# Performance work log

Measured on AMD Instinct MI355X. Metric: run time of the kernel, lower is better.

The kernel has to match this reference:

```python
import jax, jax.numpy as jnp
import numpy as np
import math

HIDDEN = 1024
HEADS = 16
HEAD_DIM = HIDDEN // HEADS
B, S = 4, 2048


def setup_inputs() -> dict:
    key = jax.random.key(0)
    ks = jax.random.split(key, 10)
    x = jax.random.normal(ks[0], (B, S, HIDDEN), dtype=jnp.float32)
    time_intervals = jax.random.uniform(ks[1], (B, S, S), dtype=jnp.float32)
    mask = jax.random.randint(ks[2], (B, 1, S, S), 0, 2, dtype=jnp.int32)
    scale = 1.0 / math.sqrt(HIDDEN)
    Wq = jax.random.normal(ks[3], (HIDDEN, HIDDEN), dtype=jnp.float32) * scale
    bq = jnp.zeros((HIDDEN,), dtype=jnp.float32)
    Wk = jax.random.normal(ks[4], (HIDDEN, HIDDEN), dtype=jnp.float32) * scale
    bk = jnp.zeros((HIDDEN,), dtype=jnp.float32)
    Wv = jax.random.normal(ks[5], (HIDDEN, HIDDEN), dtype=jnp.float32) * scale
    bv = jnp.zeros((HIDDEN,), dtype=jnp.float32)
    alpha = jnp.asarray(0.1, dtype=jnp.float32)
    return {"x": x, "time_intervals": time_intervals, "mask": mask,
            "Wq": Wq, "bq": bq, "Wk": Wk, "bk": bk, "Wv": Wv, "bv": bv,
            "alpha": alpha}


def reference(x, time_intervals, mask, Wq, bq, Wk, bk, Wv, bv, alpha):
    b, s, _ = x.shape
    # projections -> [b, heads, s, head_dim]
    def proj(W, bias):
        y = x @ W + bias
        return y.reshape(b, s, HEADS, HEAD_DIM).transpose(0, 2, 1, 3)
    Q = proj(Wq, bq)
    K = proj(Wk, bk)
    V = proj(Wv, bv)
    scores = jnp.einsum('bhqd,bhkd->bhqk', Q, K) / math.sqrt(HEAD_DIM)
    # additive time-decay bias, broadcast over heads
    scores = scores + (-jnp.abs(alpha)) * time_intervals[:, None, :, :]
    scores = jnp.where(mask == 0, jnp.float32(-1e9), scores)
    attn = jax.nn.softmax(scores, axis=-1)
    out = jnp.einsum('bhqk,bhkd->bhqd', attn, V)
    return out.transpose(0, 2, 1, 3).reshape(b, s, HIDDEN)
```

## Files before the change

kernel.cpp:

```cpp
#include <hip/hip_runtime.h>
#include <hip/hip_bf16.h>
#include <hip/hip_fp16.h>

#define BATCH 4
#define SEQ   2048
#define HID   1024
#define HEADS 16
#define HDIM  64
#define MROWS (BATCH * SEQ)
#define LOG2E 1.4426950408889634f
#define SCL   (LOG2E / 8.0f)

typedef _Float16 v8h __attribute__((ext_vector_type(8)));
typedef _Float16 v4h __attribute__((ext_vector_type(4)));
typedef _Float16 v2h __attribute__((ext_vector_type(2)));
typedef float    v4f __attribute__((ext_vector_type(4)));
typedef int      v4i __attribute__((ext_vector_type(4)));

#define MFMA16(a, b, c) __builtin_amdgcn_mfma_f32_16x16x32_f16((a), (b), (c), 0, 0, 0)
#define MFMA16K16(a, b, c) __builtin_amdgcn_mfma_f32_16x16x16f16((a), (b), (c), 0, 0, 0)

__device__ inline int pk2(float a, float b) {
    return __builtin_bit_cast(int, __builtin_amdgcn_cvt_pkrtz(a, b));
}

__device__ __forceinline__ void async16(const void* g, void* l) {
    __builtin_amdgcn_global_load_lds(
        (const __attribute__((address_space(1))) unsigned int*)g,
        (__attribute__((address_space(3))) unsigned int*)l, 16, 0, 0);
}

#define SWZ(row, chunk) (((row) * 64) + ((((chunk) ^ ((row) & 7))) * 8))

__global__ __launch_bounds__(256) void cvt_x(const float* __restrict__ x,
                                             _Float16* __restrict__ xb) {
    int i = blockIdx.x * 256 + threadIdx.x;
    const float4* xp = (const float4*)x;
    float4 a = xp[2 * i];
    float4 b = xp[2 * i + 1];
    v4i o;
    o[0] = pk2(a.x, a.y); o[1] = pk2(a.z, a.w);
    o[2] = pk2(b.x, b.y); o[3] = pk2(b.z, b.w);
    ((v4i*)xb)[i] = o;
}

__global__ __launch_bounds__(256) void transw(const float* __restrict__ W0,
                                              const float* __restrict__ W1,
                                              const float* __restrict__ W2,
                                              _Float16* __restrict__ Wt) {
    const float* W = (blockIdx.z == 0) ? W0 : (blockIdx.z == 1 ? W1 : W2);
    _Float16* dst = Wt + (size_t)blockIdx.z * HID * HID;
    __shared__ float t[32][33];
    int bx = blockIdx.x * 32, by = blockIdx.y * 32;
    int tx = threadIdx.x, ty = threadIdx.y;
#pragma unroll
    for (int i = 0; i < 4; i++)
        t[ty + i * 8][tx] = W[(size_t)(by + ty + i * 8) * HID + bx + tx];
    __syncthreads();
#pragma unroll
    for (int i = 0; i < 4; i++)
        dst[(size_t)(bx + ty + i * 8) * HID + by + tx] = (_Float16)t[tx][ty + i * 8];
}

__global__ __launch_bounds__(256) void mkbias(const float* __restrict__ tiv,
                                              const int* __restrict__ msk,
                                              const float* __restrict__ alphap,
                                              _Float16* __restrict__ biasT) {
    __shared__ _Float16 L[16 * 264];
    const int b = blockIdx.z, Q16 = blockIdx.y, kc0 = blockIdx.x * 256;
    const int tid = threadIdx.x;
    const float ca = -fabsf(alphap[0]) * LOG2E;
    const int prow = tid >> 6;
    const int pcol = (tid & 63) * 4;
#pragma unroll
    for (int pi = 0; pi < 4; pi++) {
        int r = pi * 4 + prow;
        size_t g = ((size_t)b * SEQ + Q16 * 16 + r) * SEQ + kc0 + pcol;
        float4 tv = *(const float4*)(tiv + g);
        int4   mv = *(const int4*)(msk + g);
        float f0 = mv.x ? ca * tv.x : -57344.0f;
        float f1 = mv.y ? ca * tv.y : -57344.0f;
        float f2 = mv.z ? ca * tv.z : -57344.0f;
        float f3 = mv.w ? ca * tv.w : -57344.0f;
        int2 o; o.x = pk2(f0, f1); o.y = pk2(f2, f3);
        *(int2*)&L[r * 264 + pcol] = o;
    }
    __syncthreads();
    const int lane = tid & 63, tq = tid >> 6;
#pragma unroll
    for (int it = 0; it < 4; it++) {
        int K16i = it * 4 + tq;
        int kl = K16i * 16 + (lane >> 4) * 4;
        int qr = lane & 15;
        int2 v = *(const int2*)&L[qr * 264 + kl];
        size_t o = ((((size_t)b * 128 + (kc0 >> 4) + K16i) * 128 + Q16) * 64 + lane) * 4;
        *(int2*)&biasT[o] = v;
    }
}

__global__ __launch_bounds__(256) void gemm_qkv(
    const _Float16* __restrict__ xb, const _Float16* __restrict__ wt,
    const float* __restrict__ bq, const float* __restrict__ bk,
    const float* __restrict__ bv,
    _Float16* __restrict__ Qb, _Float16* __restrict__ Kb, _Float16* __restrict__ Vtb) {
    const int mode = blockIdx.z;
    const _Float16* w = wt + (size_t)mode * HID * HID;
    __shared__ _Float16 As[128 * 64];
    __shared__ _Float16 Bs[128 * 64];
    const int tid = threadIdx.x;
    const int wv = tid >> 6, lane = tid & 63;
    const int quad = lane >> 4, l15 = lane & 15;
    const int wr = wv >> 1, wc = wv & 1;
    const int m0 = blockIdx.y * 128;
    const int n0 = blockIdx.x * 128;

    v4f acc[4][4];
#pragma unroll
    for (int i = 0; i < 4; i++)
#pragma unroll
        for (int j = 0; j < 4; j++) acc[i][j] = (v4f){0.f, 0.f, 0.f, 0.f};

    const int srow = lane >> 3;
    const int schk = lane & 7;
    const _Float16* Ag = xb + (size_t)m0 * HID;
    const _Float16* Bg = w + (size_t)n0 * HID;

    for (int k0 = 0; k0 < HID; k0 += 64) {
        __syncthreads();
#pragma unroll
        for (int i = 0; i < 4; i++) {
            int ra = wv * 32 + i * 8 + srow;
            int ca = schk ^ (ra & 7);
            async16(Ag + (size_t)ra * HID + k0 + ca * 8, &As[(wv * 32 + i * 8) * 64]);
            async16(Bg + (size_t)ra * HID + k0 + ca * 8, &Bs[(wv * 32 + i * 8) * 64]);
        }
        __syncthreads();
#pragma unroll
        for (int kc = 0; kc < 2; kc++) {
            v8h af[4], bf[4];
#pragma unroll
            for (int t = 0; t < 4; t++) {
                af[t] = *(const v8h*)&As[SWZ(wr * 64 + t * 16 + l15, kc * 4 + quad)];
                bf[t] = *(const v8h*)&Bs[SWZ(wc * 64 + t * 16 + l15, kc * 4 + quad)];
            }
#pragma unroll
            for (int tm = 0; tm < 4; tm++)
#pragma unroll
                for (int tn = 0; tn < 4; tn++)
                    acc[tm][tn] = MFMA16(af[tm], bf[tn], acc[tm][tn]);
        }
    }

    const float* pb = (mode == 0) ? bq : (mode == 1 ? bk : bv);
    const float oscl = (mode == 0) ? SCL : 1.0f;
#pragma unroll
    for (int tm = 0; tm < 4; tm++) {
#pragma unroll
        for (int tn = 0; tn < 4; tn++) {
            int n = n0 + wc * 64 + tn * 16 + l15;
            float bval = pb[n];
            int h = n >> 6, d = n & 63;
#pragma unroll
            for (int r = 0; r < 4; r++) {
                int m = m0 + wr * 64 + tm * 16 + quad * 4 + r;
                int b = m >> 11, s = m & 2047;
                _Float16 hv = (_Float16)((acc[tm][tn][r] + bval) * oscl);
                if (mode == 2) {
                    Vtb[(((size_t)(b * HEADS + h) * HDIM + d) * SEQ) + s] = hv;
                } else {
                    _Float16* dst = (mode == 0) ? Qb : Kb;
                    dst[((size_t)(b * HEADS + h) * SEQ + s) * HDIM + d] = hv;
                }
            }
        }
    }
}

__global__ __launch_bounds__(256, 4) void attn(
    const _Float16* __restrict__ Qb, const _Float16* __restrict__ Kb,
    const _Float16* __restrict__ Vtb, const _Float16* __restrict__ biasT,
    float* __restrict__ out) {
    const int wg  = (blockIdx.y << 4) | blockIdx.x;
    const int nid = ((wg & 7) << 7) | (wg >> 3);
    const int bh = nid >> 4;
    const int qt = nid & 15;
    const int b = bh >> 4, h = bh & 15;
    const int tid = threadIdx.x;
    const int wv = tid >> 6, lane = tid & 63;
    const int quad = lane >> 4, l15 = lane & 15;

    __shared__ _Float16 Ks[2][64 * 64];
    __shared__ _Float16 Vs[2][64 * 64];

    const int q0 = qt * 128 + wv * 32;
    const int Q16a = q0 >> 4;

    const _Float16* Qp = Qb + (size_t)(b * HEADS + h) * SEQ * HDIM;
    const _Float16* Kp = Kb + (size_t)(b * HEADS + h) * SEQ * HDIM;
    const _Float16* Vp = Vtb + (size_t)(b * HEADS + h) * HDIM * SEQ;
    const _Float16* Bbase = biasT + (size_t)b * 128 * 128 * 64 * 4;

    v8h qf[2][2];
#pragma unroll
    for (int tm = 0; tm < 2; tm++)
#pragma unroll
        for (int kc = 0; kc < 2; kc++)
            qf[tm][kc] = *(const v8h*)&Qp[(size_t)(q0 + tm * 16 + l15) * HDIM + kc * 32 + quad * 8];

    v4f oacc[2][4];
#pragma unroll
    for (int i = 0; i < 2; i++)
#pragma unroll
        for (int j = 0; j < 4; j++) oacc[i][j] = (v4f){0.f, 0.f, 0.f, 0.f};
    float lsum[2] = {0.f, 0.f};

    const int srow = lane >> 3, schk = lane & 7;

#define STAGE(buf_, key0_)                                                  \
    {                                                                       \
        _Pragma("unroll")                                                   \
        for (int i_ = 0; i_ < 2; i_++) {                                    \
            int r_ = wv * 16 + i_ * 8 + srow;                               \
            int c_ = schk ^ (r_ & 7);                                       \
            async16(Kp + (size_t)((key0_) + r_) * HDIM + c_ * 8,            \
                    &Ks[buf_][(wv * 16 + i_ * 8) * 64]);                    \
            async16(Vp + (size_t)r_ * SEQ + (key0_) + c_ * 8,               \
                    &Vs[buf_][(wv * 16 + i_ * 8) * 64]);                    \
        }                                                                   \
    }

#define BLOAD(key0_)                                                        \
    {                                                                       \
        _Pragma("unroll")                                                   \
        for (int nt_ = 0; nt_ < 4; nt_++)                                   \
            _Pragma("unroll")                                               \
            for (int tm_ = 0; tm_ < 2; tm_++)                               \
                bl[nt_][tm_] = *(const int2*)&Bbase[((((size_t)((key0_) >> 4) + nt_) * 128 + Q16a + tm_) * 64 + lane) * 4]; \
    }

    int2 bl[4][2];
    STAGE(0, 0)
    BLOAD(0)
    __syncthreads();

    for (int kt = 0; kt < SEQ / 64; kt++) {
        const int cur = kt & 1;
        const int key0 = kt * 64;

        v4f sacc[4][2];
#pragma unroll
        for (int nt = 0; nt < 4; nt++)
#pragma unroll
            for (int tm = 0; tm < 2; tm++) {
                v4h bv = __builtin_bit_cast(v4h, bl[nt][tm]);
                sacc[nt][tm] = (v4f){(float)bv[0], (float)bv[1], (float)bv[2], (float)bv[3]};
            }

        if (kt + 1 < SEQ / 64) {
            STAGE(cur ^ 1, key0 + 64)
            BLOAD(key0 + 64)
        }

#pragma unroll
        for (int kc = 0; kc < 2; kc++) {
            v8h kfr[4];
#pragma unroll
            for (int nt = 0; nt < 4; nt++)
                kfr[nt] = *(const v8h*)&Ks[cur][SWZ(nt * 16 + l15, kc * 4 + quad)];
#pragma unroll
            for (int nt = 0; nt < 4; nt++)
#pragma unroll
                for (int tm = 0; tm < 2; tm++)
                    sacc[nt][tm] = MFMA16(kfr[nt], qf[tm][kc], sacc[nt][tm]);
        }

        int2 pfr[4][2];
#pragma unroll
        for (int nt = 0; nt < 4; nt++)
#pragma unroll
            for (int tm = 0; tm < 2; tm++) {
                float p0 = __builtin_amdgcn_exp2f(sacc[nt][tm][0]);
                float p1 = __builtin_amdgcn_exp2f(sacc[nt][tm][1]);
                float p2 = __builtin_amdgcn_exp2f(sacc[nt][tm][2]);
                float p3 = __builtin_amdgcn_exp2f(sacc[nt][tm][3]);
                int2 pkv;
                pkv.x = pk2(p0, p1);
                pkv.y = pk2(p2, p3);
                lsum[tm] += (p0 + p1) + (p2 + p3);
                pfr[nt][tm] = pkv;
            }

#pragma unroll
        for (int g = 0; g < 4; g++) {
            v4h vfr[4];
#pragma unroll
            for (int nt = 0; nt < 4; nt++) {
                int row = nt * 16 + l15;
                int cc = g * 2 + (quad >> 1);
                vfr[nt] = *(const v4h*)&Vs[cur][row * 64 + ((cc ^ (row & 7)) * 8) + (quad & 1) * 4];
            }
#pragma unroll
            for (int tm = 0; tm < 2; tm++) {
                v4h pa = __builtin_bit_cast(v4h, pfr[g][tm]);
#pragma unroll
                for (int nt = 0; nt < 4; nt++)
                    oacc[tm][nt] = MFMA16K16(pa, vfr[nt], oacc[tm][nt]);
            }
        }

        __syncthreads();
    }

#undef STAGE
#undef BLOAD

#pragma unroll
    for (int tm = 0; tm < 2; tm++) {
        float lt = lsum[tm];
        lt += __shfl_xor(lt, 16);
        lt += __shfl_xor(lt, 32);
        float inv[4];
#pragma unroll
        for (int r = 0; r < 4; r++)
            inv[r] = 1.0f / __shfl(lt, quad * 4 + r);
#pragma unroll
        for (int nt = 0; nt < 4; nt++)
#pragma unroll
            for (int r = 0; r < 4; r++) {
                int q = q0 + tm * 16 + quad * 4 + r;
                int d = nt * 16 + l15;
                out[((size_t)b * SEQ + q) * HID + h * HDIM + d] = oacc[tm][nt][r] * inv[r];
            }
    }
}

extern "C" void kernel_launch(void* const* d_in, const int* in_sizes, int n_in,
                              void* d_out, int out_size, void* d_ws, size_t ws_size,
                              hipStream_t stream) {
    const float* x    = (const float*)d_in[0];
    const float* tiv  = (const float*)d_in[1];
    const int*   msk  = (const int*)d_in[2];
    const float* Wq   = (const float*)d_in[3];
    const float* bq   = (const float*)d_in[4];
    const float* Wk   = (const float*)d_in[5];
    const float* bk   = (const float*)d_in[6];
    const float* Wv   = (const float*)d_in[7];
    const float* bv   = (const float*)d_in[8];
    const float* alp  = (const float*)d_in[9];

    char* ws = (char*)d_ws;
    const size_t XB_OFF = 0;
    const size_t WT_OFF = XB_OFF + (size_t)MROWS * HID * 2;
    const size_t Q_OFF  = WT_OFF + (size_t)3 * HID * HID * 2;
    const size_t K_OFF  = Q_OFF + (size_t)MROWS * HID * 2;
    const size_t V_OFF  = K_OFF + (size_t)MROWS * HID * 2;
    const size_t B_OFF  = V_OFF + (size_t)MROWS * HID * 2;

    _Float16* xb   = (_Float16*)(ws + XB_OFF);
    _Float16* wt   = (_Float16*)(ws + WT_OFF);
    _Float16* Qb   = (_Float16*)(ws + Q_OFF);
    _Float16* Kb   = (_Float16*)(ws + K_OFF);
    _Float16* Vtb  = (_Float16*)(ws + V_OFF);
    _Float16* bias = (_Float16*)(ws + B_OFF);

    cvt_x<<<MROWS * HID / (256 * 8), 256, 0, stream>>>(x, xb);
    dim3 tb(32, 8);
    transw<<<dim3(32, 32, 3), tb, 0, stream>>>(Wq, Wk, Wv, wt);
    mkbias<<<dim3(SEQ / 256, SEQ / 16, BATCH), 256, 0, stream>>>(tiv, msk, alp, bias);
    gemm_qkv<<<dim3(HID / 128, MROWS / 128, 3), 256, 0, stream>>>(
        xb, wt, bq, bk, bv, Qb, Kb, Vtb);
    attn<<<dim3(SEQ / 128, BATCH * HEADS), 256, 0, stream>>>(Qb, Kb, Vtb, bias,
                                                             (float*)d_out);
}
```

Measured before the change: 392.9 us.

## Merge prep kernels and overlap bias build with QKV GEMM; add MFMA priority hints

Folds the x conversion and the weight transposes into one launch, and the QKV GEMM and the mask/time bias construction into another. Both merges use a flattened block index with a branch on it, which cuts launches from five to three. The memory-bound bias blocks can then run alongside the compute-bound GEMM blocks instead of after them. It also wraps the MFMA loops in the GEMM and attention kernels with s_setprio to raise wave priority during matrix math. The risks are that the shared-memory footprint is the larger of the two branches, and the priority hints may disturb scheduling.

Measured after the change: 448.8 us. 14.2% more time.

```diff
diff --git a/kernel.cpp b/kernel.cpp
--- a/kernel.cpp
+++ b/kernel.cpp
@@ -32,146 +32,157 @@
 
 #define SWZ(row, chunk) (((row) * 64) + ((((chunk) ^ ((row) & 7))) * 8))
 
-__global__ __launch_bounds__(256) void cvt_x(const float* __restrict__ x,
-                                             _Float16* __restrict__ xb) {
-    int i = blockIdx.x * 256 + threadIdx.x;
-    const float4* xp = (const float4*)x;
-    float4 a = xp[2 * i];
-    float4 b = xp[2 * i + 1];
-    v4i o;
-    o[0] = pk2(a.x, a.y); o[1] = pk2(a.z, a.w);
-    o[2] = pk2(b.x, b.y); o[3] = pk2(b.z, b.w);
-    ((v4i*)xb)[i] = o;
-}
-
-__global__ __launch_bounds__(256) void transw(const float* __restrict__ W0,
-                                              const float* __restrict__ W1,
-                                              const float* __restrict__ W2,
-                                              _Float16* __restrict__ Wt) {
-    const float* W = (blockIdx.z == 0) ? W0 : (blockIdx.z == 1 ? W1 : W2);
-    _Float16* dst = Wt + (size_t)blockIdx.z * HID * HID;
+__global__ __launch_bounds__(256) void prep(
+    const float* __restrict__ x, _Float16* __restrict__ xb,
+    const float* __restrict__ W0, const float* __restrict__ W1,
+    const float* __restrict__ W2, _Float16* __restrict__ Wt) {
     __shared__ float t[32][33];
-    int bx = blockIdx.x * 32, by = blockIdx.y * 32;
-    int tx = threadIdx.x, ty = threadIdx.y;
-#pragma unroll
-    for (int i = 0; i < 4; i++)
-        t[ty + i * 8][tx] = W[(size_t)(by + ty + i * 8) * HID + bx + tx];
-    __syncthreads();
-#pragma unroll
-    for (int i = 0; i < 4; i++)
-        dst[(size_t)(bx + ty + i * 8) * HID + by + tx] = (_Float16)t[tx][ty + i * 8];
-}
-
-__global__ __launch_bounds__(256) void mkbias(const float* __restrict__ tiv,
-                                              const int* __restrict__ msk,
-                                              const float* __restrict__ alphap,
-                                              _Float16* __restrict__ biasT) {
-    __shared__ _Float16 L[16 * 264];
-    const int b = blockIdx.z, Q16 = blockIdx.y, kc0 = blockIdx.x * 256;
+    const int bid = blockIdx.x;
     const int tid = threadIdx.x;
-    const float ca = -fabsf(alphap[0]) * LOG2E;
-    const int prow = tid >> 6;
-    const int pcol = (tid & 63) * 4;
-#pragma unroll
-    for (int pi = 0; pi < 4; pi++) {
-        int r = pi * 4 + prow;
-        size_t g = ((size_t)b * SEQ + Q16 * 16 + r) * SEQ + kc0 + pcol;
-        float4 tv = *(const float4*)(tiv + g);
-        int4   mv = *(const int4*)(msk + g);
-        float f0 = mv.x ? ca * tv.x : -57344.0f;
-        float f1 = mv.y ? ca * tv.y : -57344.0f;
-        float f2 = mv.z ? ca * tv.z : -57344.0f;
-        float f3 = mv.w ? ca * tv.w : -57344.0f;
-        int2 o; o.x = pk2(f0, f1); o.y = pk2(f2, f3);
-        *(int2*)&L[r * 264 + pcol] = o;
-    }
-    __syncthreads();
-    const int lane = tid & 63, tq = tid >> 6;
-#pragma unroll
-    for (int it = 0; it < 4; it++) {
-        int K16i = it * 4 + tq;
-        int kl = K16i * 16 + (lane >> 4) * 4;
-        int qr = lane & 15;
-        int2 v = *(const int2*)&L[qr * 264 + kl];
-        size_t o = ((((size_t)b * 128 + (kc0 >> 4) + K16i) * 128 + Q16) * 64 + lane) * 4;
-        *(int2*)&biasT[o] = v;
-    }
-}
-
-__global__ __launch_bounds__(256) void gemm_qkv(
+    if (bid < 4096) {
+        int i = bid * 256 + tid;
+        const float4* xp = (const float4*)x;
+        float4 a = xp[2 * i];
+        float4 b = xp[2 * i + 1];
+        v4i o;
+        o[0] = pk2(a.x, a.y); o[1] = pk2(a.z, a.w);
+        o[2] = pk2(b.x, b.y); o[3] = pk2(b.z, b.w);
+        ((v4i*)xb)[i] = o;
+    } else {
+        int tt = bid - 4096;
+        int z = tt >> 10;
+        int rem = tt & 1023;
+        const float* W = (z == 0) ? W0 : (z == 1 ? W1 : W2);
+        _Float16* dst = Wt + (size_t)z * HID * HID;
+        int bx = (rem & 31) * 32, by = (rem >> 5) * 32;
+        int tx = tid & 31, ty = tid >> 5;
+#pragma unroll
+        for (int i = 0; i < 4; i++)
+            t[ty + i * 8][tx] = W[(size_t)(by + ty + i * 8) * HID + bx + tx];
+        __syncthreads();
+#pragma unroll
+        for (int i = 0; i < 4; i++)
+            dst[(size_t)(bx + ty + i * 8) * HID + by + tx] = (_Float16)t[tx][ty + i * 8];
+    }
+}
+
+__global__ __launch_bounds__(256) void gemm_bias(
     const _Float16* __restrict__ xb, const _Float16* __restrict__ wt,
     const float* __restrict__ bq, const float* __restrict__ bk,
     const float* __restrict__ bv,
-    _Float16* __restrict__ Qb, _Float16* __restrict__ Kb, _Float16* __restrict__ Vtb) {
-    const int mode = blockIdx.z;
-    const _Float16* w = wt + (size_t)mode * HID * HID;
-    __shared__ _Float16 As[128 * 64];
-    __shared__ _Float16 Bs[128 * 64];
+    _Float16* __restrict__ Qb, _Float16* __restrict__ Kb, _Float16* __restrict__ Vtb,
+    const float* __restrict__ tiv, const int* __restrict__ msk,
+    const float* __restrict__ alphap, _Float16* __restrict__ biasT) {
+    __shared__ _Float16 smem[2 * 128 * 64];
+    const int bid = blockIdx.x;
     const int tid = threadIdx.x;
-    const int wv = tid >> 6, lane = tid & 63;
-    const int quad = lane >> 4, l15 = lane & 15;
-    const int wr = wv >> 1, wc = wv & 1;
-    const int m0 = blockIdx.y * 128;
-    const int n0 = blockIdx.x * 128;
-
-    v4f acc[4][4];
-#pragma unroll
-    for (int i = 0; i < 4; i++)
-#pragma unroll
-        for (int j = 0; j < 4; j++) acc[i][j] = (v4f){0.f, 0.f, 0.f, 0.f};
-
-    const int srow = lane >> 3;
-    const int schk = lane & 7;
-    const _Float16* Ag = xb + (size_t)m0 * HID;
-    const _Float16* Bg = w + (size_t)n0 * HID;
-
-    for (int k0 = 0; k0 < HID; k0 += 64) {
+
+    if (bid < 1536) {
+        const int mode = bid >> 9;
+        const int within = bid & 511;
+        const int n0 = (within & 7) * 128;
+        const int m0 = (within >> 3) * 128;
+        const _Float16* w = wt + (size_t)mode * HID * HID;
+        _Float16* As = smem;
+        _Float16* Bs = smem + 128 * 64;
+        const int wv = tid >> 6, lane = tid & 63;
+        const int quad = lane >> 4, l15 = lane & 15;
+        const int wr = wv >> 1, wc = wv & 1;
+
+        v4f acc[4][4];
+#pragma unroll
+        for (int i = 0; i < 4; i++)
+#pragma unroll
+            for (int j = 0; j < 4; j++) acc[i][j] = (v4f){0.f, 0.f, 0.f, 0.f};
+
+        const int srow = lane >> 3;
+        const int schk = lane & 7;
+        const _Float16* Ag = xb + (size_t)m0 * HID;
+        const _Float16* Bg = w + (size_t)n0 * HID;
+
+        for (int k0 = 0; k0 < HID; k0 += 64) {
+            __syncthreads();
+#pragma unroll
+            for (int i = 0; i < 4; i++) {
+                int ra = wv * 32 + i * 8 + srow;
+                int ca = schk ^ (ra & 7);
+                async16(Ag + (size_t)ra * HID + k0 + ca * 8, &As[(wv * 32 + i * 8) * 64]);
+                async16(Bg + (size_t)ra * HID + k0 + ca * 8, &Bs[(wv * 32 + i * 8) * 64]);
+            }
+            __syncthreads();
+#pragma unroll
+            for (int kc = 0; kc < 2; kc++) {
+                v8h af[4], bf[4];
+#pragma unroll
+                for (int t = 0; t < 4; t++) {
+                    af[t] = *(const v8h*)&As[SWZ(wr * 64 + t * 16 + l15, kc * 4 + quad)];
+                    bf[t] = *(const v8h*)&Bs[SWZ(wc * 64 + t * 16 + l15, kc * 4 + quad)];
+                }
+                __builtin_amdgcn_s_setprio(1);
+#pragma unroll
+                for (int tm = 0; tm < 4; tm++)
+#pragma unroll
+                    for (int tn = 0; tn < 4; tn++)
+                        acc[tm][tn] = MFMA16(af[tm], bf[tn], acc[tm][tn]);
+                __builtin_amdgcn_s_setprio(0);
+            }
+        }
+
+        const float* pb = (mode == 0) ? bq : (mode == 1 ? bk : bv);
+        const float oscl = (mode == 0) ? SCL : 1.0f;
+#pragma unroll
+        for (int tm = 0; tm < 4; tm++) {
+#pragma unroll
+            for (int tn = 0; tn < 4; tn++) {
+                int n = n0 + wc * 64 + tn * 16 + l15;
+                float bval = pb[n];
+                int h = n >> 6, d = n & 63;
+#pragma unroll
+                for (int r = 0; r < 4; r++) {
+                    int m = m0 + wr * 64 + tm * 16 + quad * 4 + r;
+                    int b = m >> 11, s = m & 2047;
+                    _Float16 hv = (_Float16)((acc[tm][tn][r] + bval) * oscl);
+                    if (mode == 2) {
+                        Vtb[(((size_t)(b * HEADS + h) * HDIM + d) * SEQ) + s] = hv;
+                    } else {
+                        _Float16* dst = (mode == 0) ? Qb : Kb;
+                        dst[((size_t)(b * HEADS + h) * SEQ + s) * HDIM + d] = hv;
+                    }
+                }
+            }
+        }
+    } else {
+        const int t = bid - 1536;
+        const int kc0 = (t & 7) * 256;
+        const int Q16 = (t >> 3) & 127;
+        const int b = t >> 10;
+        _Float16* L = smem;
+        const float ca = -fabsf(alphap[0]) * LOG2E;
+        const int prow = tid >> 6;
+        const int pcol = (tid & 63) * 4;
+#pragma unroll
+        for (int pi = 0; pi < 4; pi++) {
+            int r = pi * 4 + prow;
+            size_t g = ((size_t)b * SEQ + Q16 * 16 + r) * SEQ + kc0 + pcol;
+            float4 tv = *(const float4*)(tiv + g);
+            int4   mv = *(const int4*)(msk + g);
+            float f0 = mv.x ? ca * tv.x : -57344.0f;
+            float f1 = mv.y ? ca * tv.y : -57344.0f;
+            float f2 = mv.z ? ca * tv.z : -57344.0f;
+            float f3 = mv.w ? ca * tv.w : -57344.0f;
+            int2 o; o.x = pk2(f0, f1); o.y = pk2(f2, f3);
+            *(int2*)&L[r * 264 + pcol] = o;
+        }
         __syncthreads();
-#pragma unroll
-        for (int i = 0; i < 4; i++) {
-            int ra = wv * 32 + i * 8 + srow;
-            int ca = schk ^ (ra & 7);
-            async16(Ag + (size_t)ra * HID + k0 + ca * 8, &As[(wv * 32 + i * 8) * 64]);
-            async16(Bg + (size_t)ra * HID + k0 + ca * 8, &Bs[(wv * 32 + i * 8) * 64]);
-        }
-        __syncthreads();
-#pragma unroll
-        for (int kc = 0; kc < 2; kc++) {
-            v8h af[4], bf[4];
-#pragma unroll
-            for (int t = 0; t < 4; t++) {
-                af[t] = *(const v8h*)&As[SWZ(wr * 64 + t * 16 + l15, kc * 4 + quad)];
-                bf[t] = *(const v8h*)&Bs[SWZ(wc * 64 + t * 16 + l15, kc * 4 + quad)];
-            }
-#pragma unroll
-            for (int tm = 0; tm < 4; tm++)
-#pragma unroll
-                for (int tn = 0; tn < 4; tn++)
-                    acc[tm][tn] = MFMA16(af[tm], bf[tn], acc[tm][tn]);
-        }
-    }
-
-    const float* pb = (mode == 0) ? bq : (mode == 1 ? bk : bv);
-    const float oscl = (mode == 0) ? SCL : 1.0f;
-#pragma unroll
-    for (int tm = 0; tm < 4; tm++) {
-#pragma unroll
-        for (int tn = 0; tn < 4; tn++) {
-            int n = n0 + wc * 64 + tn * 16 + l15;
-            float bval = pb[n];
-            int h = n >> 6, d = n & 63;
-#pragma unroll
-            for (int r = 0; r < 4; r++) {
-                int m = m0 + wr * 64 + tm * 16 + quad * 4 + r;
-                int b = m >> 11, s = m & 2047;
-                _Float16 hv = (_Float16)((acc[tm][tn][r] + bval) * oscl);
-                if (mode == 2) {
-                    Vtb[(((size_t)(b * HEADS + h) * HDIM + d) * SEQ) + s] = hv;
-                } else {
-                    _Float16* dst = (mode == 0) ? Qb : Kb;
-                    dst[((size_t)(b * HEADS + h) * SEQ + s) * HDIM + d] = hv;
-                }
-            }
+        const int lane = tid & 63, tq = tid >> 6;
+#pragma unroll
+        for (int it = 0; it < 4; it++) {
+            int K16i = it * 4 + tq;
+            int kl = K16i * 16 + (lane >> 4) * 4;
+            int qr = lane & 15;
+            int2 v = *(const int2*)&L[qr * 264 + kl];
+            size_t o = ((((size_t)b * 128 + (kc0 >> 4) + K16i) * 128 + Q16) * 64 + lane) * 4;
+            *(int2*)&biasT[o] = v;
         }
     }
 }
@@ -267,11 +278,13 @@
 #pragma unroll
             for (int nt = 0; nt < 4; nt++)
                 kfr[nt] = *(const v8h*)&Ks[cur][SWZ(nt * 16 + l15, kc * 4 + quad)];
+            __builtin_amdgcn_s_setprio(1);
 #pragma unroll
             for (int nt = 0; nt < 4; nt++)
 #pragma unroll
                 for (int tm = 0; tm < 2; tm++)
                     sacc[nt][tm] = MFMA16(kfr[nt], qf[tm][kc], sacc[nt][tm]);
+            __builtin_amdgcn_s_setprio(0);
         }
 
         int2 pfr[4][2];
@@ -299,6 +312,7 @@
                 int cc = g * 2 + (quad >> 1);
                 vfr[nt] = *(const v4h*)&Vs[cur][row * 64 + ((cc ^ (row & 7)) * 8) + (quad & 1) * 4];
             }
+            __builtin_amdgcn_s_setprio(1);
 #pragma unroll
             for (int tm = 0; tm < 2; tm++) {
                 v4h pa = __builtin_bit_cast(v4h, pfr[g][tm]);
@@ -306,6 +320,7 @@
                 for (int nt = 0; nt < 4; nt++)
                     oacc[tm][nt] = MFMA16K16(pa, vfr[nt], oacc[tm][nt]);
             }
+            __builtin_amdgcn_s_setprio(0);
         }
 
         __syncthreads();
@@ -363,12 +378,9 @@
     _Float16* Vtb  = (_Float16*)(ws + V_OFF);
     _Float16* bias = (_Float16*)(ws + B_OFF);
 
-    cvt_x<<<MROWS * HID / (256 * 8), 256, 0, stream>>>(x, xb);
-    dim3 tb(32, 8);
-    transw<<<dim3(32, 32, 3), tb, 0, stream>>>(Wq, Wk, Wv, wt);
-    mkbias<<<dim3(SEQ / 256, SEQ / 16, BATCH), 256, 0, stream>>>(tiv, msk, alp, bias);
-    gemm_qkv<<<dim3(HID / 128, MROWS / 128, 3), 256, 0, stream>>>(
-        xb, wt, bq, bk, bv, Qb, Kb, Vtb);
+    prep<<<4096 + 3072, 256, 0, stream>>>(x, xb, Wq, Wk, Wv, wt);
+    gemm_bias<<<1536 + 4096, 256, 0, stream>>>(xb, wt, bq, bk, bv, Qb, Kb, Vtb,
+                                               tiv, msk, alp, bias);
     attn<<<dim3(SEQ / 128, BATCH * HEADS), 256, 0, stream>>>(Qb, Kb, Vtb, bias,
                                                              (float*)d_out);
 }
```
